# Kernel optimization log

Measured on AMD Instinct MI355X. Metric: run time of the kernel, lower is better.

Reference implementation:

```python
import jax, jax.numpy as jnp
import numpy as np

B, L, N_ELECS, N_HID = 2048, 16, 256, 64
N_SITES = L * L  # 256


def setup_inputs() -> dict:
    key = jax.random.key(0)
    k1, k2, k3 = jax.random.split(key, 3)
    # spin configurations in {-1, +1}: one electron per site at half filling
    x = 2 * jax.random.randint(k1, (B, N_SITES), 0, 2, dtype=jnp.int32) - 1
    orbitals_mf = 0.1 * jax.random.normal(k2, (2 * N_SITES, N_ELECS), dtype=jnp.float32)
    orbitals_hf = 0.1 * jax.random.normal(k3, (2 * N_SITES, N_HID), dtype=jnp.float32)
    return {"x": x, "orbitals_mf": orbitals_mf, "orbitals_hf": orbitals_hf}


def reference(x, orbitals_mf, orbitals_hf):
    # x: (B, N_sites) int in {-1,+1}
    n_sites = x.shape[-1]
    # (2N, n_elecs + n_hid)
    orbitals_full = jnp.concatenate([orbitals_mf, orbitals_hf], axis=1)
    spin_up = (x == 1)   # (B, N)
    spin_dn = (x == -1)  # (B, N)
    mask = jnp.concatenate([spin_up, spin_dn], axis=-1).astype(jnp.int32)  # (B, 2N)
    # top_k over the boolean mask: indices of occupied spin-orbitals,
    # ties (equal values) resolved by lowest index, matching jax.lax.top_k on bools
    _, idx = jax.lax.top_k(mask, n_sites)  # (B, N)
    # gather orbital rows: (B, N, n_elecs + n_hid)
    return orbitals_full[idx, :]
```

## Files before the change

kernel.cpp:

```cpp
#include <hip/hip_runtime.h>


#define NBATCH 2048
#define NS 256
#define NMF 256
#define NHF 64
#define NROW 320

typedef float v4f __attribute__((ext_vector_type(4)));

__global__ __launch_bounds__(256) void gather_orbitals(
    const int* __restrict__ x,
    const float* __restrict__ mf,
    const float* __restrict__ hf,
    float* __restrict__ out)
{
    __shared__ int src[NS];
    __shared__ int wtot[4];

    const int b    = blockIdx.x;
    const int tid  = threadIdx.x;
    const int wave = tid >> 6;
    const int lane = tid & 63;

    const int xv = x[(size_t)b * NS + tid];
    const bool up = (xv == 1);
    const unsigned long long m = __ballot(up);
    const int lane_ex = __popcll(m & ((1ull << lane) - 1ull));
    if (lane == 0) wtot[wave] = __popcll(m);
    __syncthreads();

    int woff = 0, nup = 0;
#pragma unroll
    for (int w = 0; w < 4; ++w) {
        const int c = wtot[w];
        if (w < wave) woff += c;
        nup += c;
    }
    const int upex = woff + lane_ex;
    const int dest = up ? upex : (nup + (tid - upex));
    src[dest] = up ? tid : (NS + tid);
    __syncthreads();

    float* outb = out + (size_t)b * NS * NROW;
    const int j16 = lane >> 4;
    const int l16 = lane & 15;

    for (int ss = 0; ss < 8; ++ss) {
        const int rbase = ss * 32 + wave * 8;

        int s[8];
#pragma unroll
        for (int k = 0; k < 8; ++k) s[k] = src[rbase + k];

        v4f vm[8];
#pragma unroll
        for (int k = 0; k < 8; ++k)
            vm[k] = ((const v4f*)(mf + (size_t)s[k] * NMF))[lane];

        const int sh0 = src[rbase + j16];
        const int sh1 = src[rbase + 4 + j16];
        const v4f vh0 = ((const v4f*)(hf + (size_t)sh0 * NHF))[l16];
        const v4f vh1 = ((const v4f*)(hf + (size_t)sh1 * NHF))[l16];

#pragma unroll
        for (int k = 0; k < 4; ++k)
            ((v4f*)(outb + (size_t)(rbase + k) * NROW))[lane] = vm[k];
        ((v4f*)(outb + (size_t)(rbase + j16) * NROW + NMF))[l16] = vh0;
#pragma unroll
        for (int k = 4; k < 8; ++k)
            ((v4f*)(outb + (size_t)(rbase + k) * NROW))[lane] = vm[k];
        ((v4f*)(outb + (size_t)(rbase + 4 + j16) * NROW + NMF))[l16] = vh1;
    }
}

extern "C" void kernel_launch(void* const* d_in, const int* in_sizes, int n_in,
                              void* d_out, int out_size, void* d_ws, size_t ws_size,
                              hipStream_t stream) {
    const int*   x  = (const int*)d_in[0];
    const float* mf = (const float*)d_in[1];
    const float* hf = (const float*)d_in[2];
    float* out = (float*)d_out;

    gather_orbitals<<<dim3(NBATCH), dim3(256), 0, stream>>>(x, mf, hf, out);
}
```

Before: 127.6 us.

## Process four batch rows per 1024-thread block with 16 waves sharing rows

Result: slower. 131.7 us (+3.2%).

```diff
diff --git a/kernel.cpp b/kernel.cpp
--- a/kernel.cpp
+++ b/kernel.cpp
@@ -6,71 +6,75 @@
 #define NMF 256
 #define NHF 64
 #define NROW 320
+#define BPB 4
+#define THREADS 1024
 
 typedef float v4f __attribute__((ext_vector_type(4)));
 
-__global__ __launch_bounds__(256) void gather_orbitals(
+__global__ __launch_bounds__(THREADS) void gather_orbitals(
     const int* __restrict__ x,
     const float* __restrict__ mf,
     const float* __restrict__ hf,
     float* __restrict__ out)
 {
-    __shared__ int src[NS];
-    __shared__ int wtot[4];
+    __shared__ int srcs[BPB * NS];
+    __shared__ int wtot[16];
 
-    const int b    = blockIdx.x;
+    const int bstart = blockIdx.x * BPB;
     const int tid  = threadIdx.x;
-    const int wave = tid >> 6;
+    const int q    = tid >> 8;
+    const int t    = tid & 255;
+    const int gw   = tid >> 6;
+    const int wl   = gw & 3;
     const int lane = tid & 63;
 
-    const int xv = x[(size_t)b * NS + tid];
+    const int xv = x[(size_t)(bstart + q) * NS + t];
     const bool up = (xv == 1);
     const unsigned long long m = __ballot(up);
     const int lane_ex = __popcll(m & ((1ull << lane) - 1ull));
-    if (lane == 0) wtot[wave] = __popcll(m);
+    if (lane == 0) wtot[gw] = __popcll(m);
     __syncthreads();
 
     int woff = 0, nup = 0;
 #pragma unroll
     for (int w = 0; w < 4; ++w) {
-        const int c = wtot[w];
-        if (w < wave) woff += c;
+        const int c = wtot[q * 4 + w];
+        if (w < wl) woff += c;
         nup += c;
     }
     const int upex = woff + lane_ex;
-    const int dest = up ? upex : (nup + (tid - upex));
-    src[dest] = up ? tid : (NS + tid);
+    const int dest = up ? upex : (nup + (t - upex));
+    srcs[q * NS + dest] = up ? t : (NS + t);
     __syncthreads();
 
-    float* outb = out + (size_t)b * NS * NROW;
     const int j16 = lane >> 4;
     const int l16 = lane & 15;
 
-    for (int ss = 0; ss < 8; ++ss) {
-        const int rbase = ss * 32 + wave * 8;
+#pragma unroll 1
+    for (int qq = 0; qq < BPB; ++qq) {
+        const int* srcq = srcs + qq * NS;
+        float* outq = out + (size_t)(bstart + qq) * NS * NROW;
 
-        int s[8];
+#pragma unroll 2
+        for (int c = 0; c < 4; ++c) {
+            const int rbase = gw * 16 + c * 4;
+
+            int s[4];
 #pragma unroll
-        for (int k = 0; k < 8; ++k) s[k] = src[rbase + k];
+            for (int k = 0; k < 4; ++k) s[k] = srcq[rbase + k];
+            const int sh = srcq[rbase + j16];
 
-        v4f vm[8];
+            v4f vm[4];
 #pragma unroll
-        for (int k = 0; k < 8; ++k)
-            vm[k] = ((const v4f*)(mf + (size_t)s[k] * NMF))[lane];
-
-        const int sh0 = src[rbase + j16];
-        const int sh1 = src[rbase + 4 + j16];
-        const v4f vh0 = ((const v4f*)(hf + (size_t)sh0 * NHF))[l16];
-        const v4f vh1 = ((const v4f*)(hf + (size_t)sh1 * NHF))[l16];
+            for (int k = 0; k < 4; ++k)
+                vm[k] = ((const v4f*)(mf + (size_t)s[k] * NMF))[lane];
+            const v4f vh = ((const v4f*)(hf + (size_t)sh * NHF))[l16];
 
 #pragma unroll
-        for (int k = 0; k < 4; ++k)
-            ((v4f*)(outb + (size_t)(rbase + k) * NROW))[lane] = vm[k];
-        ((v4f*)(outb + (size_t)(rbase + j16) * NROW + NMF))[l16] = vh0;
-#pragma unroll
-        for (int k = 4; k < 8; ++k)
-            ((v4f*)(outb + (size_t)(rbase + k) * NROW))[lane] = vm[k];
-        ((v4f*)(outb + (size_t)(rbase + 4 + j16) * NROW + NMF))[l16] = vh1;
+            for (int k = 0; k < 4; ++k)
+                ((v4f*)(outq + (size_t)(rbase + k) * NROW))[lane] = vm[k];
+            ((v4f*)(outq + (size_t)(rbase + j16) * NROW + NMF))[l16] = vh;
+        }
     }
 }
 
@@ -82,5 +86,5 @@
     const float* hf = (const float*)d_in[2];
     float* out = (float*)d_out;
 
-    gather_orbitals<<<dim3(NBATCH), dim3(256), 0, stream>>>(x, mf, hf, out);
+    gather_orbitals<<<dim3(NBATCH / BPB), dim3(THREADS), 0, stream>>>(x, mf, hf, out);
 }
```
